# Kernel optimization log

Hardware: AMD Instinct MI355X
Metric: run time of the kernel (lower is better)

The kernel has to match this reference:

```python
import jax, jax.numpy as jnp
import numpy as np

N = 50000
IN_C, H_DIM, Z_DIM = 256, 128, 64
E = 1600000


def gcn_conv(x, edge_index, W, b):
    # PyG GCNConv: out = D^{-1/2} (A + I) D^{-1/2} (x @ W) + b
    n = x.shape[0]
    src = jnp.concatenate([edge_index[0], jnp.arange(n)])  # add self-loops
    dst = jnp.concatenate([edge_index[1], jnp.arange(n)])
    deg = jax.ops.segment_sum(jnp.ones_like(dst, dtype=x.dtype), dst, num_segments=n)
    dinv = jnp.where(deg > 0, jax.lax.rsqrt(deg), 0.0)
    norm = dinv[src] * dinv[dst]                 # [E+n]
    xw = x @ W                                   # [n, out_c] dense GEMM first (out_c <= in_c)
    msg = xw[src] * norm[:, None]                # gather + scale
    out = jax.ops.segment_sum(msg, dst, num_segments=n)  # scatter-add
    return out + b


def setup_inputs() -> dict:
    key = jax.random.key(0)
    ks = jax.random.split(key, 8)
    glorot = lambda k, fi, fo: jax.random.uniform(k, (fi, fo), jnp.float32, -1.0, 1.0) * np.sqrt(6.0 / (fi + fo))
    return {
        "x": jax.random.normal(ks[0], (N, IN_C), jnp.float32),
        "W_h": glorot(ks[1], IN_C, H_DIM),
        "b_h": jnp.zeros((H_DIM,), jnp.float32),
        "W_mu": glorot(ks[2], H_DIM, Z_DIM),
        "b_mu": jnp.zeros((Z_DIM,), jnp.float32),
        "W_ls": glorot(ks[3], H_DIM, Z_DIM),
        "b_ls": jnp.zeros((Z_DIM,), jnp.float32),
        "edge_index": jax.random.randint(ks[4], (2, E), 0, N, jnp.int64) if jax.config.read('jax_enable_x64') else jax.random.randint(ks[4], (2, E), 0, N, jnp.int32),
    }


def reference(x, W_h, b_h, W_mu, b_mu, W_ls, b_ls, edge_index):
    h = jax.nn.relu(gcn_conv(x, edge_index, W_h, b_h))
    mu = gcn_conv(h, edge_index, W_mu, b_mu)
    logstd = gcn_conv(h, edge_index, W_ls, b_ls)
    return (mu, logstd)
```

## Files before the change

kernel.cpp:

```cpp
#include <hip/hip_runtime.h>

#define INC 256
#define HD 128
#define ZD 64
#define NPB 196
#define NB  256

typedef __attribute__((ext_vector_type(8))) short bf16x8;
typedef __attribute__((ext_vector_type(4))) float f32x4;

static __device__ __forceinline__ unsigned short f2b(float f) {
    unsigned u = __builtin_bit_cast(unsigned, f);
    unsigned r = (u + 0x7fffu + ((u >> 16) & 1u)) >> 16;
    return (unsigned short)r;
}
static __device__ __forceinline__ float b_lo(unsigned u) {
    return __builtin_bit_cast(float, u << 16);
}
static __device__ __forceinline__ float b_hi(unsigned u) {
    return __builtin_bit_cast(float, u & 0xffff0000u);
}


__global__ __launch_bounds__(256) void k_bhist(const int* __restrict__ dst,
                                               int* __restrict__ bhist, int E) {
    __shared__ int h[NB];
    h[threadIdx.x] = 0;
    __syncthreads();
    for (int i = blockIdx.x * blockDim.x + threadIdx.x; i < E; i += gridDim.x * blockDim.x)
        atomicAdd(&h[dst[i] / NPB], 1);
    __syncthreads();
    int v = h[threadIdx.x];
    if (v) atomicAdd(&bhist[threadIdx.x], v);
}

__global__ __launch_bounds__(NB) void k_bscan(const int* __restrict__ bhist,
                                              int* __restrict__ bbase,
                                              int* __restrict__ bcur) {
    __shared__ int s[NB];
    int t = threadIdx.x;
    int v = bhist[t];
    s[t] = v;
    __syncthreads();
    for (int o = 1; o < NB; o <<= 1) {
        int x = (t >= o) ? s[t - o] : 0;
        __syncthreads();
        s[t] += x;
        __syncthreads();
    }
    bbase[t] = s[t] - v;
    bcur[t] = s[t] - v;
}

__global__ __launch_bounds__(256) void k_bscatter(const int* __restrict__ src,
                                                  const int* __restrict__ dst,
                                                  int* __restrict__ bcur,
                                                  unsigned* __restrict__ pairp, int E) {
    __shared__ int lcnt[NB];
    __shared__ int lbase[NB];
    const int t = threadIdx.x;
    lcnt[t] = 0;
    __syncthreads();
    const int c0 = blockIdx.x * 1024;
    unsigned u_[4]; int r_[4], b_[4], m_ = 0;
#pragma unroll
    for (int k = 0; k < 4; k++) {
        int i = c0 + k * 256 + t;
        if (i < E) {
            int dd = dst[i];
            int b = dd / NPB;
            b_[k] = b;
            u_[k] = (unsigned)src[i] | ((unsigned)(dd - b * NPB) << 16);
            r_[k] = atomicAdd(&lcnt[b], 1);
            m_ = k + 1;
        }
    }
    __syncthreads();
    lbase[t] = lcnt[t] ? atomicAdd(&bcur[t], lcnt[t]) : 0;
    __syncthreads();
    for (int k = 0; k < m_; k++)
        pairp[lbase[b_[k]] + r_[k]] = u_[k];
}


__global__ __launch_bounds__(256) void k_build(const unsigned* __restrict__ pairp,
                                               const int* __restrict__ bbase,
                                               const int* __restrict__ bhist,
                                               int* __restrict__ cnt,
                                               float* __restrict__ dinv,
                                               int* __restrict__ rowstart,
                                               int* __restrict__ csr, int n) {
    __shared__ int lc[NPB];
    __shared__ int cur[NPB];
    __shared__ int s[256];
    const int t = threadIdx.x;
    const int b = blockIdx.x;
    const int node0 = b * NPB;
    const int np = min(NPB, n - node0);

    for (int r = t; r < NPB; r += 256) lc[r] = 0;
    __syncthreads();
    const int lo = bbase[b], hi = lo + bhist[b];
    for (int i = lo + t; i < hi; i += 256)
        atomicAdd(&lc[pairp[i] >> 16], 1);
    __syncthreads();

    int v = (t < NPB) ? lc[t] : 0;
    s[t] = v;
    __syncthreads();
    for (int o = 1; o < 256; o <<= 1) {
        int x = (t >= o) ? s[t - o] : 0;
        __syncthreads();
        s[t] += x;
        __syncthreads();
    }
    if (t < np) {
        int rs = lo + s[t] - v;
        rowstart[node0 + t] = rs;
        cnt[node0 + t] = v;
        dinv[node0 + t] = rsqrtf((float)(v + 1));
        cur[t] = rs;
    }
    __syncthreads();
    for (int i = lo + t; i < hi; i += 256) {
        unsigned u = pairp[i];
        int p = atomicAdd(&cur[u >> 16], 1);
        csr[p] = (int)(u & 0xffffu);
    }
}


template <int K, int SPLITB>
__global__ void k_pack(const float* __restrict__ Wa, const float* __restrict__ Wb,
                       unsigned short* __restrict__ Wp) {
    int idx = blockIdx.x * 256 + threadIdx.x;
    int j = idx & 7, lane = (idx >> 3) & 63, c = (idx >> 9) & 7, s = idx >> 12;
    int k = s * 32 + (lane >> 4) * 8 + j;
    int col = c * 16 + (lane & 15);
    float v;
    if (!SPLITB) v = Wa[k * 128 + col];
    else v = (col < 64) ? Wa[k * 64 + col] : Wb[k * 64 + (col - 64)];
    Wp[idx] = f2b(v);
}


template <int K, int AF32>
__global__ __launch_bounds__(256) void k_mgemm(const void* __restrict__ Av,
                                               const unsigned short* __restrict__ Wp,
                                               unsigned short* __restrict__ Y, int n) {
    const int lane = threadIdx.x & 63;
    const int w = threadIdx.x >> 6;
    const int rowbase = blockIdx.x * 64 + w * 16;
    int arow = rowbase + (lane & 15);
    if (arow >= n) arow = n - 1;
    const int kgrp = lane >> 4;

    f32x4 acc[8] = {};
#pragma unroll
    for (int s = 0; s < K / 32; s++) {
        bf16x8 a;
        if (AF32) {
            const float* ap = (const float*)Av + (size_t)arow * K + s * 32 + kgrp * 8;
            float4 f0 = *reinterpret_cast<const float4*>(ap);
            float4 f1 = *reinterpret_cast<const float4*>(ap + 4);
            a[0] = (short)f2b(f0.x); a[1] = (short)f2b(f0.y);
            a[2] = (short)f2b(f0.z); a[3] = (short)f2b(f0.w);
            a[4] = (short)f2b(f1.x); a[5] = (short)f2b(f1.y);
            a[6] = (short)f2b(f1.z); a[7] = (short)f2b(f1.w);
        } else {
            a = *reinterpret_cast<const bf16x8*>((const unsigned short*)Av +
                                                 (size_t)arow * K + s * 32 + kgrp * 8);
        }
        const bf16x8* bp = reinterpret_cast<const bf16x8*>(Wp) + ((size_t)s * 8 * 64 + lane);
#pragma unroll
        for (int c = 0; c < 8; c++) {
            bf16x8 b = bp[c * 64];
            acc[c] = __builtin_amdgcn_mfma_f32_16x16x32_bf16(a, b, acc[c], 0, 0, 0);
        }
    }
    const int r0 = rowbase + (lane >> 4) * 4;
    const int col = lane & 15;
#pragma unroll
    for (int c = 0; c < 8; c++) {
#pragma unroll
        for (int r = 0; r < 4; r++) {
            int rr = r0 + r;
            if (rr < n) Y[(size_t)rr * 128 + c * 16 + col] = f2b(acc[c][r]);
        }
    }
}


#define EDGE(i) \
    { int s##i = csr[base + k + i]; \
      float ds = dinv[s##i]; \
      unsigned u = in[(size_t)s##i * 64 + lane]; \
      ax += ds * b_lo(u); ay += ds * b_hi(u); }

template <int RELU, int SPLIT>
__global__ __launch_bounds__(256) void k_agg(const unsigned* __restrict__ in,
                                             const int* __restrict__ csr,
                                             const int* __restrict__ rowstart,
                                             const int* __restrict__ cnt,
                                             const float* __restrict__ dinv,
                                             const float* __restrict__ b0,
                                             const float* __restrict__ b1,
                                             void* __restrict__ out0v,
                                             void* __restrict__ out1v, int n) {
    const int wid = threadIdx.x >> 6;
    const int lane = threadIdx.x & 63;
    const int d = blockIdx.x * 4 + wid;
    if (d >= n) return;

    const float dd = dinv[d];
    unsigned su = in[(size_t)d * 64 + lane];
    float ax = dd * b_lo(su), ay = dd * b_hi(su);

    const int base = rowstart[d];
    const int m = cnt[d];
    int k = 0;
    for (; k + 7 < m; k += 8) {
        int s0 = csr[base + k],     s1 = csr[base + k + 1];
        int s2 = csr[base + k + 2], s3 = csr[base + k + 3];
        int s4 = csr[base + k + 4], s5 = csr[base + k + 5];
        int s6 = csr[base + k + 6], s7 = csr[base + k + 7];
        float e0 = dinv[s0], e1 = dinv[s1], e2 = dinv[s2], e3 = dinv[s3];
        float e4 = dinv[s4], e5 = dinv[s5], e6 = dinv[s6], e7 = dinv[s7];
        unsigned u0 = in[(size_t)s0 * 64 + lane];
        unsigned u1 = in[(size_t)s1 * 64 + lane];
        unsigned u2 = in[(size_t)s2 * 64 + lane];
        unsigned u3 = in[(size_t)s3 * 64 + lane];
        unsigned u4 = in[(size_t)s4 * 64 + lane];
        unsigned u5 = in[(size_t)s5 * 64 + lane];
        unsigned u6 = in[(size_t)s6 * 64 + lane];
        unsigned u7 = in[(size_t)s7 * 64 + lane];
        ax += e0 * b_lo(u0) + e1 * b_lo(u1) + e2 * b_lo(u2) + e3 * b_lo(u3)
            + e4 * b_lo(u4) + e5 * b_lo(u5) + e6 * b_lo(u6) + e7 * b_lo(u7);
        ay += e0 * b_hi(u0) + e1 * b_hi(u1) + e2 * b_hi(u2) + e3 * b_hi(u3)
            + e4 * b_hi(u4) + e5 * b_hi(u5) + e6 * b_hi(u6) + e7 * b_hi(u7);
    }
    for (; k + 3 < m; k += 4) {
        int s0 = csr[base + k],     s1 = csr[base + k + 1];
        int s2 = csr[base + k + 2], s3 = csr[base + k + 3];
        float e0 = dinv[s0], e1 = dinv[s1], e2 = dinv[s2], e3 = dinv[s3];
        unsigned u0 = in[(size_t)s0 * 64 + lane];
        unsigned u1 = in[(size_t)s1 * 64 + lane];
        unsigned u2 = in[(size_t)s2 * 64 + lane];
        unsigned u3 = in[(size_t)s3 * 64 + lane];
        ax += e0 * b_lo(u0) + e1 * b_lo(u1) + e2 * b_lo(u2) + e3 * b_lo(u3);
        ay += e0 * b_hi(u0) + e1 * b_hi(u1) + e2 * b_hi(u2) + e3 * b_hi(u3);
    }
    for (; k < m; k++) EDGE(0);
    ax *= dd; ay *= dd;

    if (!SPLIT) {
        float2 b = reinterpret_cast<const float2*>(b0)[lane];
        ax += b.x; ay += b.y;
        if (RELU) { ax = fmaxf(ax, 0.f); ay = fmaxf(ay, 0.f); }
        ((unsigned*)out0v)[(size_t)d * 64 + lane] =
            (unsigned)f2b(ax) | ((unsigned)f2b(ay) << 16);
    } else {
        if (lane < 32) {
            float2 b = reinterpret_cast<const float2*>(b0)[lane];
            reinterpret_cast<float2*>(out0v)[(size_t)d * 32 + lane] =
                make_float2(ax + b.x, ay + b.y);
        } else {
            float2 b = reinterpret_cast<const float2*>(b1)[lane - 32];
            reinterpret_cast<float2*>(out1v)[(size_t)d * 32 + (lane - 32)] =
                make_float2(ax + b.x, ay + b.y);
        }
    }
}


extern "C" void kernel_launch(void* const* d_in, const int* in_sizes, int n_in,
                              void* d_out, int out_size, void* d_ws, size_t ws_size,
                              hipStream_t stream) {
    const float* x    = (const float*)d_in[0];
    const float* W_h  = (const float*)d_in[1];
    const float* b_h  = (const float*)d_in[2];
    const float* W_mu = (const float*)d_in[3];
    const float* b_mu = (const float*)d_in[4];
    const float* W_ls = (const float*)d_in[5];
    const float* b_ls = (const float*)d_in[6];
    const int*   ei   = (const int*)d_in[7];

    const int E = in_sizes[7] / 2;
    const int n = in_sizes[0] / INC;
    const int* src = ei;
    const int* dst = ei + E;
    float* out = (float*)d_out;

    char* p = (char*)d_ws;
    auto carve = [&](size_t bytes) {
        void* r = (void*)p;
        p += (bytes + 255) & ~(size_t)255;
        return r;
    };
    unsigned short* xw  = (unsigned short*)carve((size_t)n * HD * 2);
    unsigned short* h   = (unsigned short*)carve((size_t)n * HD * 2);
    unsigned short* wp1 = (unsigned short*)carve((size_t)INC * HD * 2);
    unsigned short* wp2 = (unsigned short*)carve((size_t)HD * HD * 2);
    float* dinv     = (float*)carve((size_t)n * 4);
    int*   cnt      = (int*)carve((size_t)n * 4);
    int*   rowstart = (int*)carve((size_t)n * 4);
    int*   bhist    = (int*)carve((size_t)NB * 4);
    int*   bbase    = (int*)carve((size_t)NB * 4);
    int*   bcur     = (int*)carve((size_t)NB * 4);
    unsigned* pairp = (unsigned*)carve((size_t)E * 4);
    int*   csr      = (int*)carve((size_t)E * 4);

    hipMemsetAsync(bhist, 0, (size_t)NB * 4, stream);

    k_bhist<<<256, 256, 0, stream>>>(dst, bhist, E);
    k_bscan<<<1, NB, 0, stream>>>(bhist, bbase, bcur);
    k_bscatter<<<(E + 1023) / 1024, 256, 0, stream>>>(src, dst, bcur, pairp, E);
    k_build<<<NB, 256, 0, stream>>>(pairp, bbase, bhist, cnt, dinv, rowstart, csr, n);

    k_pack<INC, 0><<<INC * HD / 256, 256, 0, stream>>>(W_h, nullptr, wp1);
    k_pack<HD, 1><<<HD * HD / 256, 256, 0, stream>>>(W_mu, W_ls, wp2);

    k_mgemm<INC, 1><<<(n + 63) / 64, 256, 0, stream>>>(x, wp1, xw, n);
    k_agg<1, 0><<<(n + 3) / 4, 256, 0, stream>>>((const unsigned*)xw, csr, rowstart, cnt,
                                                 dinv, b_h, nullptr, h, nullptr, n);
    k_mgemm<HD, 0><<<(n + 63) / 64, 256, 0, stream>>>(h, wp2, xw, n);
    k_agg<0, 1><<<(n + 3) / 4, 256, 0, stream>>>((const unsigned*)xw, csr, rowstart, cnt,
                                                 dinv, b_mu, b_ls, out, out + (size_t)n * ZD, n);
}
```

Measured before the change: 318.6 us.

## Fold source-degree scaling into GEMM epilogue and store byte offsets in CSR

The GEMM epilogue now multiplies each output row by dinv of that row, so the aggregation no longer gathers dinv for every neighbour and becomes a plain sum of pre-scaled rows. The CSR stores precomputed byte offsets (index<<8), and the aggregation reads them as wave-uniform scalars via readfirstlane, unrolled 16 wide to keep more gathers in flight. This removes one random load and one multiply per edge and per-lane address arithmetic. In exchange the pre-scaled values are rounded to bf16 after scaling, which changes numerics slightly.

```diff
diff --git a/kernel.cpp b/kernel.cpp
--- a/kernel.cpp
+++ b/kernel.cpp
@@ -89,7 +89,7 @@
                                                int* __restrict__ cnt,
                                                float* __restrict__ dinv,
                                                int* __restrict__ rowstart,
-                                               int* __restrict__ csr, int n) {
+                                               unsigned* __restrict__ csr, int n) {
     __shared__ int lc[NPB];
     __shared__ int cur[NPB];
     __shared__ int s[256];
@@ -125,7 +125,7 @@
     for (int i = lo + t; i < hi; i += 256) {
         unsigned u = pairp[i];
         int p = atomicAdd(&cur[u >> 16], 1);
-        csr[p] = (int)(u & 0xffffu);
+        csr[p] = (u & 0xffffu) << 8;
     }
 }
 
@@ -147,6 +147,7 @@
 template <int K, int AF32>
 __global__ __launch_bounds__(256) void k_mgemm(const void* __restrict__ Av,
                                                const unsigned short* __restrict__ Wp,
+                                               const float* __restrict__ rowscale,
                                                unsigned short* __restrict__ Y, int n) {
     const int lane = threadIdx.x & 63;
     const int w = threadIdx.x >> 6;
@@ -180,26 +181,26 @@
     }
     const int r0 = rowbase + (lane >> 4) * 4;
     const int col = lane & 15;
+    float sc[4];
+#pragma unroll
+    for (int r = 0; r < 4; r++) {
+        int rr = r0 + r;
+        sc[r] = (rr < n) ? rowscale[rr] : 0.f;
+    }
 #pragma unroll
     for (int c = 0; c < 8; c++) {
 #pragma unroll
         for (int r = 0; r < 4; r++) {
             int rr = r0 + r;
-            if (rr < n) Y[(size_t)rr * 128 + c * 16 + col] = f2b(acc[c][r]);
-        }
-    }
-}
-
-
-#define EDGE(i) \
-    { int s##i = csr[base + k + i]; \
-      float ds = dinv[s##i]; \
-      unsigned u = in[(size_t)s##i * 64 + lane]; \
-      ax += ds * b_lo(u); ay += ds * b_hi(u); }
+            if (rr < n) Y[(size_t)rr * 128 + c * 16 + col] = f2b(acc[c][r] * sc[r]);
+        }
+    }
+}
+
 
 template <int RELU, int SPLIT>
 __global__ __launch_bounds__(256) void k_agg(const unsigned* __restrict__ in,
-                                             const int* __restrict__ csr,
+                                             const unsigned* __restrict__ csr,
                                              const int* __restrict__ rowstart,
                                              const int* __restrict__ cnt,
                                              const float* __restrict__ dinv,
@@ -214,43 +215,39 @@
 
     const float dd = dinv[d];
     unsigned su = in[(size_t)d * 64 + lane];
-    float ax = dd * b_lo(su), ay = dd * b_hi(su);
-
-    const int base = rowstart[d];
-    const int m = cnt[d];
+    float ax = b_lo(su), ay = b_hi(su);
+
+    const int base = __builtin_amdgcn_readfirstlane(rowstart[d]);
+    const int m = __builtin_amdgcn_readfirstlane(cnt[d]);
+    const char* inb = (const char*)in;
+    const int l4 = lane << 2;
+
     int k = 0;
-    for (; k + 7 < m; k += 8) {
-        int s0 = csr[base + k],     s1 = csr[base + k + 1];
-        int s2 = csr[base + k + 2], s3 = csr[base + k + 3];
-        int s4 = csr[base + k + 4], s5 = csr[base + k + 5];
-        int s6 = csr[base + k + 6], s7 = csr[base + k + 7];
-        float e0 = dinv[s0], e1 = dinv[s1], e2 = dinv[s2], e3 = dinv[s3];
-        float e4 = dinv[s4], e5 = dinv[s5], e6 = dinv[s6], e7 = dinv[s7];
-        unsigned u0 = in[(size_t)s0 * 64 + lane];
-        unsigned u1 = in[(size_t)s1 * 64 + lane];
-        unsigned u2 = in[(size_t)s2 * 64 + lane];
-        unsigned u3 = in[(size_t)s3 * 64 + lane];
-        unsigned u4 = in[(size_t)s4 * 64 + lane];
-        unsigned u5 = in[(size_t)s5 * 64 + lane];
-        unsigned u6 = in[(size_t)s6 * 64 + lane];
-        unsigned u7 = in[(size_t)s7 * 64 + lane];
-        ax += e0 * b_lo(u0) + e1 * b_lo(u1) + e2 * b_lo(u2) + e3 * b_lo(u3)
-            + e4 * b_lo(u4) + e5 * b_lo(u5) + e6 * b_lo(u6) + e7 * b_lo(u7);
-        ay += e0 * b_hi(u0) + e1 * b_hi(u1) + e2 * b_hi(u2) + e3 * b_hi(u3)
-            + e4 * b_hi(u4) + e5 * b_hi(u5) + e6 * b_hi(u6) + e7 * b_hi(u7);
+    for (; k + 15 < m; k += 16) {
+        unsigned u[16];
+#pragma unroll
+        for (int j = 0; j < 16; j++) {
+            unsigned off = (unsigned)__builtin_amdgcn_readfirstlane((int)csr[base + k + j]);
+            u[j] = *reinterpret_cast<const unsigned*>(inb + off + l4);
+        }
+#pragma unroll
+        for (int j = 0; j < 16; j++) { ax += b_lo(u[j]); ay += b_hi(u[j]); }
     }
     for (; k + 3 < m; k += 4) {
-        int s0 = csr[base + k],     s1 = csr[base + k + 1];
-        int s2 = csr[base + k + 2], s3 = csr[base + k + 3];
-        float e0 = dinv[s0], e1 = dinv[s1], e2 = dinv[s2], e3 = dinv[s3];
-        unsigned u0 = in[(size_t)s0 * 64 + lane];
-        unsigned u1 = in[(size_t)s1 * 64 + lane];
-        unsigned u2 = in[(size_t)s2 * 64 + lane];
-        unsigned u3 = in[(size_t)s3 * 64 + lane];
-        ax += e0 * b_lo(u0) + e1 * b_lo(u1) + e2 * b_lo(u2) + e3 * b_lo(u3);
-        ay += e0 * b_hi(u0) + e1 * b_hi(u1) + e2 * b_hi(u2) + e3 * b_hi(u3);
-    }
-    for (; k < m; k++) EDGE(0);
+        unsigned u[4];
+#pragma unroll
+        for (int j = 0; j < 4; j++) {
+            unsigned off = (unsigned)__builtin_amdgcn_readfirstlane((int)csr[base + k + j]);
+            u[j] = *reinterpret_cast<const unsigned*>(inb + off + l4);
+        }
+#pragma unroll
+        for (int j = 0; j < 4; j++) { ax += b_lo(u[j]); ay += b_hi(u[j]); }
+    }
+    for (; k < m; k++) {
+        unsigned off = (unsigned)__builtin_amdgcn_readfirstlane((int)csr[base + k]);
+        unsigned u = *reinterpret_cast<const unsigned*>(inb + off + l4);
+        ax += b_lo(u); ay += b_hi(u);
+    }
     ax *= dd; ay *= dd;
 
     if (!SPLIT) {
@@ -308,7 +305,7 @@
     int*   bbase    = (int*)carve((size_t)NB * 4);
     int*   bcur     = (int*)carve((size_t)NB * 4);
     unsigned* pairp = (unsigned*)carve((size_t)E * 4);
-    int*   csr      = (int*)carve((size_t)E * 4);
+    unsigned* csr   = (unsigned*)carve((size_t)E * 4);
 
     hipMemsetAsync(bhist, 0, (size_t)NB * 4, stream);
 
@@ -320,10 +317,10 @@
     k_pack<INC, 0><<<INC * HD / 256, 256, 0, stream>>>(W_h, nullptr, wp1);
     k_pack<HD, 1><<<HD * HD / 256, 256, 0, stream>>>(W_mu, W_ls, wp2);
 
-    k_mgemm<INC, 1><<<(n + 63) / 64, 256, 0, stream>>>(x, wp1, xw, n);
+    k_mgemm<INC, 1><<<(n + 63) / 64, 256, 0, stream>>>(x, wp1, dinv, xw, n);
     k_agg<1, 0><<<(n + 3) / 4, 256, 0, stream>>>((const unsigned*)xw, csr, rowstart, cnt,
                                                  dinv, b_h, nullptr, h, nullptr, n);
-    k_mgemm<HD, 0><<<(n + 63) / 64, 256, 0, stream>>>(h, wp2, xw, n);
+    k_mgemm<HD, 0><<<(n + 63) / 64, 256, 0, stream>>>(h, wp2, dinv, xw, n);
     k_agg<0, 1><<<(n + 3) / 4, 256, 0, stream>>>((const unsigned*)xw, csr, rowstart, cnt,
                                                  dinv, b_mu, b_ls, out, out + (size_t)n * ZD, n);
 }
```

Result: faster. 310.4 us (-2.6%).
